# Kernel optimization log

Hardware: AMD Instinct MI355X
Metric: run time of the kernel (lower is better)

The kernel has to match this reference:

```python
import jax, jax.numpy as jnp
import numpy as np

B, C, H, W = 8, 256, 48, 48
CK = 64  # C // k
WSCALE = 0.3 / np.sqrt(C)  # keep exp(QK^T) finite (original has no 1/sqrt(d) scaling)


def conv1x1(x, w, b):
    # x: (B,C,H,W), w: (O,C,1,1), b: (O,) -> (B,O,H,W)
    return jnp.einsum('bchw,oc->bohw', x, w[:, :, 0, 0]) + b[None, :, None, None]


def setup_inputs() -> dict:
    key = jax.random.key(0)
    ks = jax.random.split(key, 6)
    x = jax.random.normal(ks[0], (B, C, H, W), dtype=jnp.float32)
    qw = jax.random.normal(ks[1], (CK, C, 1, 1), dtype=jnp.float32) * WSCALE
    kw = jax.random.normal(ks[2], (CK, C, 1, 1), dtype=jnp.float32) * WSCALE
    vw = jax.random.normal(ks[3], (C, C, 1, 1), dtype=jnp.float32) * (1.0 / np.sqrt(C))
    gw = jax.random.normal(ks[4], (C, C, 1, 1), dtype=jnp.float32) * (1.0 / np.sqrt(C))
    zk = jnp.zeros((CK,), dtype=jnp.float32)
    zc = jnp.zeros((C,), dtype=jnp.float32)
    return {
        'x': x,
        'query_weight': qw, 'query_bias': zk,
        'key_weight': kw, 'key_bias': zk,
        'value_weight': vw, 'value_bias': zc,
        'gamma_weight': gw, 'gamma_bias': zc,
        'k': 4,
    }


def reference(x, query_weight, query_bias, key_weight, key_bias,
              value_weight, value_bias, gamma_weight, gamma_bias, k):
    b, c, h, w = x.shape
    n = h * w
    q = conv1x1(x, query_weight, query_bias).reshape(b, -1, n)   # (B,Ck,N)
    kk = conv1x1(x, key_weight, key_bias).reshape(b, -1, n)      # (B,Ck,N)
    # energy[b,i,j] = q_i . k_j  (queries on rows, no sqrt(d) scaling)
    energy = jnp.einsum('bci,bcj->bij', q, kk)                   # (B,N,N)
    energy = jnp.exp(energy)
    energy = energy / jnp.sum(energy, axis=2, keepdims=True)     # unnormalized-softmax over keys
    v = conv1x1(x, value_weight, value_bias).reshape(b, c, n)    # (B,C,N)
    # out[b,c,j] = sum_i v[b,c,i] * energy[b,i,j]  (faithful to torch.bmm(V, energy))
    out = jnp.einsum('bci,bij->bcj', v, energy).reshape(b, c, h, w)
    out = conv1x1(out, gamma_weight, gamma_bias)
    return out
```

## Files before the change

### kernel.cpp

```cpp
#include <hip/hip_runtime.h>

#define BATCH 8
#define CIN   256
#define NPIX  2304
#define CKD   64
#define NIT   (NPIX / 16)
#define NIC   (NPIX / 32)
#define NJB   (NPIX / 64)

typedef _Float16 f16;
typedef __attribute__((ext_vector_type(4))) _Float16 f16x4;
typedef __attribute__((ext_vector_type(8))) _Float16 f16x8;
typedef __attribute__((ext_vector_type(4))) float    f32x4;


__global__ __launch_bounds__(256) void cast_w(
    const float* __restrict__ qw, const float* __restrict__ kw,
    const float* __restrict__ vw, const float* __restrict__ gw,
    f16* __restrict__ Wqk, f16* __restrict__ Wv, f16* __restrict__ Wg)
{
    int idx = (blockIdx.x * 256 + threadIdx.x) * 4;
    const float* src;
    f16* dst;
    if (idx < 16384)      { src = qw + idx;           dst = Wqk + idx; }
    else if (idx < 32768) { src = kw + (idx - 16384); dst = Wqk + idx; }
    else if (idx < 98304) { src = vw + (idx - 32768); dst = Wv + (idx - 32768); }
    else                  { src = gw + (idx - 98304); dst = Wg + (idx - 98304); }
    float4 v = *(const float4*)src;
    f16x4 h = { (f16)v.x, (f16)v.y, (f16)v.z, (f16)v.w };
    *(f16x4*)dst = h;
}

__global__ __launch_bounds__(256) void cast_xT(
    const float* __restrict__ x, f16* __restrict__ xT)
{
    __shared__ float s[64][65];
    const int t = threadIdx.x;
    const int n0 = blockIdx.x * 64, c0 = blockIdx.y * 64, b = blockIdx.z;
    const float* xb = x + ((size_t)b * CIN + c0) * NPIX + n0;

    const int cl = t >> 4, ng = (t & 15) * 4;
    #pragma unroll
    for (int p = 0; p < 4; ++p) {
        float4 v = *(const float4*)(xb + (size_t)(cl + 16 * p) * NPIX + ng);
        s[cl + 16 * p][ng + 0] = v.x;
        s[cl + 16 * p][ng + 1] = v.y;
        s[cl + 16 * p][ng + 2] = v.z;
        s[cl + 16 * p][ng + 3] = v.w;
    }
    __syncthreads();
    const int nl = t >> 2, cs = (t & 3) * 16;
    f16 h[16];
    #pragma unroll
    for (int j = 0; j < 16; ++j) h[j] = (f16)s[cs + j][nl];
    f16* gp = &xT[((size_t)b * NPIX + n0 + nl) * CIN + c0 + cs];
    *(f16x8*)gp       = *(f16x8*)&h[0];
    *(f16x8*)(gp + 8) = *(f16x8*)&h[8];
}

__global__ __launch_bounds__(256) void qk_conv_mfma(
    const f16* __restrict__ xT, const f16* __restrict__ Wqk,
    const float* __restrict__ qbias, const float* __restrict__ kbias,
    f16* __restrict__ q_blk, f16* __restrict__ k_blk)
{
    __shared__ __align__(16) f16 us[32 * 136];
    const int t = threadIdx.x, w = t >> 6, lane = t & 63;
    const int quad = lane >> 4, l16 = lane & 15;
    const int wm = w & 1, wn = w >> 1;
    const int n0 = blockIdx.x * 32, b = blockIdx.y;

    const f16* bp = xT + ((size_t)b * NPIX + n0 + 16 * wn + l16) * CIN;
    const f16* ap = Wqk + (size_t)(64 * wm + l16) * CIN;

    f32x4 acc[4];
    #pragma unroll
    for (int mt = 0; mt < 4; ++mt) acc[mt] = (f32x4){0.f, 0.f, 0.f, 0.f};

    #pragma unroll
    for (int kk = 0; kk < CIN; kk += 32) {
        f16x8 bf = *(const f16x8*)(bp + kk + quad * 8);
        #pragma unroll
        for (int mt = 0; mt < 4; ++mt) {
            f16x8 af = *(const f16x8*)(ap + (size_t)mt * 16 * CIN + kk + quad * 8);
            acc[mt] = __builtin_amdgcn_mfma_f32_16x16x32_f16(af, bf, acc[mt], 0, 0, 0);
        }
    }
    const float* bias = wm ? kbias - 64 : qbias;
    #pragma unroll
    for (int mt = 0; mt < 4; ++mt) {
        int ob = 64 * wm + 16 * mt + quad * 4;
        #pragma unroll
        for (int r = 0; r < 4; ++r)
            us[(16 * wn + l16) * 136 + ob + r] = (f16)(acc[mt][r] + bias[ob + r]);
    }
    __syncthreads();
    {
        int ks2 = t >> 7, nt = (t >> 6) & 1, ln = t & 63;
        const f16* usr = &us[(nt * 16 + (ln & 15)) * 136 + ks2 * 32 + (ln >> 4) * 8];
        size_t base = (((size_t)b * NIT + (n0 >> 4) + nt) * 2 + ks2) * 512 + ln * 8;
        *(f16x8*)&q_blk[base] = *(const f16x8*)(usr);
        *(f16x8*)&k_blk[base] = *(const f16x8*)(usr + 64);
    }
}

#define ESL 136
__global__ __launch_bounds__(256) void energy_S(
    const f16* __restrict__ q_blk, const f16* __restrict__ k_blk,
    float* __restrict__ Pred)
{
    __shared__ __align__(16) f16 es[64 * ESL];
    __shared__ float red2[2][128];
    const int t    = threadIdx.x;
    const int w    = t >> 6, lane = t & 63;
    const int quad = lane >> 4, l16 = lane & 15;
    const int j0 = blockIdx.x * 64, i0 = blockIdx.y * 128, b = blockIdx.z;
    const size_t ln8 = (size_t)lane * 8;
    const f16* qb = q_blk + (size_t)b * NIT * 2 * 512 + ln8;

    f32x4 acc[8];
    #pragma unroll
    for (int mt = 0; mt < 8; ++mt) acc[mt] = (f32x4){0.f, 0.f, 0.f, 0.f};

    #pragma unroll
    for (int ks = 0; ks < 2; ++ks) {
        f16x8 bf = *(const f16x8*)(k_blk +
            (((size_t)b * NIT + (j0 >> 4) + w) * 2 + ks) * 512 + ln8);
        #pragma unroll
        for (int mt = 0; mt < 8; ++mt) {
            f16x8 af = *(const f16x8*)(qb + ((size_t)((i0 >> 4) + mt) * 2 + ks) * 512);
            acc[mt] = __builtin_amdgcn_mfma_f32_16x16x32_f16(af, bf, acc[mt], 0, 0, 0);
        }
    }

    #pragma unroll
    for (int mt = 0; mt < 8; ++mt) {
        f16x4 h = { (f16)__expf(acc[mt][0]), (f16)__expf(acc[mt][1]),
                    (f16)__expf(acc[mt][2]), (f16)__expf(acc[mt][3]) };
        *(f16x4*)&es[(16 * w + l16) * ESL + 16 * mt + quad * 4] = h;
    }
    __syncthreads();
    {
        int i = t & 127, jq = t >> 7;
        float s = 0.f;
        #pragma unroll
        for (int jj = 0; jj < 32; ++jj)
            s += (float)es[(jq * 32 + jj) * ESL + i];
        red2[jq][i] = s;
    }
    __syncthreads();
    if (t < 128)
        Pred[((size_t)blockIdx.x * BATCH + b) * NPIX + i0 + t] =
            red2[0][t] + red2[1][t];
}

__global__ __launch_bounds__(256) void reduce_S(
    const float* __restrict__ Pred, float* __restrict__ S)
{
    const size_t BN = (size_t)BATCH * NPIX;
    size_t idx = (size_t)blockIdx.x * 256 + threadIdx.x;
    float s = 0.f;
    #pragma unroll
    for (int jb = 0; jb < NJB; ++jb)
        s += Pred[(size_t)jb * BN + idx];
    S[idx] = s;
}

__global__ __launch_bounds__(256) void v_conv_mfma(
    const f16* __restrict__ xT, const f16* __restrict__ Wv,
    const float* __restrict__ vbias, const float* __restrict__ S,
    f16* __restrict__ u_blk)
{
    __shared__ __align__(16) f16 smem[9216];
    f16* As = smem;
    f16* Bs = smem + 128 * 40;
    f16* us = smem;
    const int t = threadIdx.x, w = t >> 6, lane = t & 63;
    const int quad = lane >> 4, l16 = lane & 15;
    const int wm = w & 1, wn = w >> 1;
    const int i0 = blockIdx.x * 64, c0 = blockIdx.y * 128, b = blockIdx.z;
    const int sub = t >> 2, le = t & 3;
    const f16* srcA = Wv + (size_t)(c0 + sub) * CIN + le * 8;
    const f16* srcB = xT + ((size_t)b * NPIX + i0 + sub) * CIN + le * 8;
    const int ldsw = sub * 40 + le * 8;

    f32x4 acc[4][2];
    #pragma unroll
    for (int mt = 0; mt < 4; ++mt)
        #pragma unroll
        for (int nt = 0; nt < 2; ++nt)
            acc[mt][nt] = (f32x4){0.f, 0.f, 0.f, 0.f};

    for (int kk = 0; kk < CIN; kk += 32) {
        f16x8 ta0 = *(const f16x8*)(srcA + kk);
        f16x8 ta1 = *(const f16x8*)(srcA + (size_t)64 * CIN + kk);
        f16x8 tb0 = *(const f16x8*)(srcB + kk);
        __syncthreads();
        *(f16x8*)&As[ldsw]           = ta0;
        *(f16x8*)&As[64 * 40 + ldsw] = ta1;
        *(f16x8*)&Bs[ldsw]           = tb0;
        __syncthreads();
        f16x8 af[4], bf[2];
        #pragma unroll
        for (int mt = 0; mt < 4; ++mt)
            af[mt] = *(const f16x8*)&As[(64 * wm + 16 * mt + l16) * 40 + quad * 8];
        #pragma unroll
        for (int nt = 0; nt < 2; ++nt)
            bf[nt] = *(const f16x8*)&Bs[(32 * wn + 16 * nt + l16) * 40 + quad * 8];
        #pragma unroll
        for (int mt = 0; mt < 4; ++mt)
            #pragma unroll
            for (int nt = 0; nt < 2; ++nt)
                acc[mt][nt] = __builtin_amdgcn_mfma_f32_16x16x32_f16(
                    af[mt], bf[nt], acc[mt][nt], 0, 0, 0);
    }

    __syncthreads();
    #pragma unroll
    for (int nt = 0; nt < 2; ++nt) {
        int i = 32 * wn + 16 * nt + l16;
        float is = 1.0f / S[(size_t)b * NPIX + i0 + i];
        #pragma unroll
        for (int mt = 0; mt < 4; ++mt)
            #pragma unroll
            for (int r = 0; r < 4; ++r) {
                int c = 64 * wm + 16 * mt + quad * 4 + r;
                us[c * 72 + i] = (f16)((acc[mt][nt][r] + vbias[c0 + c]) * is);
            }
    }
    __syncthreads();
    #pragma unroll
    for (int p = 0; p < 4; ++p) {
        int g  = t + 256 * p;
        int ct = g >> 7, ic = (g >> 6) & 1, ln = g & 63;
        f16x8 v = *(const f16x8*)&us[(ct * 16 + (ln & 15)) * 72 + ic * 32 + (ln >> 4) * 8];
        *(f16x8*)&u_blk[(((size_t)b * 16 + (c0 >> 4) + ct) * NIC + (i0 >> 5) + ic) * 512 + ln * 8] = v;
    }
}

__global__ __launch_bounds__(256) void fused_bmm(
    const f16* __restrict__ q_blk, const f16* __restrict__ k_blk,
    const f16* __restrict__ u_blk, f16* __restrict__ o1T)
{
    __shared__ __align__(16) f16 es[64 * 72];
    const int t = threadIdx.x, w = t >> 6, lane = t & 63;
    const int quad = lane >> 4, l16 = lane & 15;
    const int j0 = blockIdx.x * 64;
    const int ch = blockIdx.y, b = blockIdx.z;
    const size_t ln8 = (size_t)lane * 8;

    const f16* qb = q_blk + (size_t)b * NIT * 2 * 512 + ln8;
    const f16* ub = u_blk + (size_t)b * 16 * NIC * 512 + ln8;

    f16x8 kf[2];
    #pragma unroll
    for (int ks = 0; ks < 2; ++ks)
        kf[ks] = *(const f16x8*)(k_blk +
            (((size_t)b * NIT + (j0 >> 4) + w) * 2 + ks) * 512 + ln8);

    const int CT0 = ch * 8 + 2 * w;

    f32x4 acc[2][4];
    #pragma unroll
    for (int mt = 0; mt < 2; ++mt)
        #pragma unroll
        for (int jt = 0; jt < 4; ++jt)
            acc[mt][jt] = (f32x4){0.f, 0.f, 0.f, 0.f};

    for (int ic = 0; ic < NPIX / 64; ++ic) {
        f32x4 e[4];
        #pragma unroll
        for (int it = 0; it < 4; ++it) e[it] = (f32x4){0.f, 0.f, 0.f, 0.f};
        #pragma unroll
        for (int ks = 0; ks < 2; ++ks)
            #pragma unroll
            for (int it = 0; it < 4; ++it) {
                f16x8 af = *(const f16x8*)(qb + ((size_t)(ic * 4 + it) * 2 + ks) * 512);
                e[it] = __builtin_amdgcn_mfma_f32_16x16x32_f16(af, kf[ks], e[it], 0, 0, 0);
            }
        __syncthreads();
        #pragma unroll
        for (int it = 0; it < 4; ++it) {
            f16x4 h = { (f16)__expf(e[it][0]), (f16)__expf(e[it][1]),
                        (f16)__expf(e[it][2]), (f16)__expf(e[it][3]) };
            *(f16x4*)&es[(16 * w + l16) * 72 + it * 16 + quad * 4] = h;
        }
        __syncthreads();
        #pragma unroll
        for (int isub = 0; isub < 2; ++isub) {
            f16x8 af0 = *(const f16x8*)(ub + ((size_t)(CT0 + 0) * NIC + ic * 2 + isub) * 512);
            f16x8 af1 = *(const f16x8*)(ub + ((size_t)(CT0 + 1) * NIC + ic * 2 + isub) * 512);
            #pragma unroll
            for (int jt = 0; jt < 4; ++jt) {
                f16x8 bf = *(const f16x8*)&es[(16 * jt + l16) * 72 + isub * 32 + quad * 8];
                acc[0][jt] = __builtin_amdgcn_mfma_f32_16x16x32_f16(af0, bf, acc[0][jt], 0, 0, 0);
                acc[1][jt] = __builtin_amdgcn_mfma_f32_16x16x32_f16(af1, bf, acc[1][jt], 0, 0, 0);
            }
        }
    }

    #pragma unroll
    for (int mt = 0; mt < 2; ++mt) {
        int cb = ch * 128 + 32 * w + 16 * mt + quad * 4;
        #pragma unroll
        for (int jt = 0; jt < 4; ++jt) {
            int j = j0 + 16 * jt + l16;
            f16x4 h = { (f16)acc[mt][jt][0], (f16)acc[mt][jt][1],
                        (f16)acc[mt][jt][2], (f16)acc[mt][jt][3] };
            *(f16x4*)&o1T[((size_t)b * NPIX + j) * CIN + cb] = h;
        }
    }
}

__global__ __launch_bounds__(256) void gamma_conv_mfma(
    const f16* __restrict__ o1T, const f16* __restrict__ Wg,
    const float* __restrict__ gbias, float* __restrict__ out)
{
    __shared__ __align__(16) f16 As[128 * 40];
    __shared__ __align__(16) f16 Bs[64 * 40];
    const int t = threadIdx.x, w = t >> 6, lane = t & 63;
    const int quad = lane >> 4, l16 = lane & 15;
    const int wm = w & 1, wn = w >> 1;
    const int j0 = blockIdx.x * 64, o0 = blockIdx.y * 128, b = blockIdx.z;
    const int sub = t >> 2, le = t & 3;
    const f16* srcA = Wg + (size_t)(o0 + sub) * CIN + le * 8;
    const f16* srcB = o1T + ((size_t)b * NPIX + j0 + sub) * CIN + le * 8;
    const int ldsw = sub * 40 + le * 8;

    f32x4 acc[4][2];
    #pragma unroll
    for (int mt = 0; mt < 4; ++mt)
        #pragma unroll
        for (int nt = 0; nt < 2; ++nt)
            acc[mt][nt] = (f32x4){0.f, 0.f, 0.f, 0.f};

    for (int kk = 0; kk < CIN; kk += 32) {
        f16x8 ta0 = *(const f16x8*)(srcA + kk);
        f16x8 ta1 = *(const f16x8*)(srcA + (size_t)64 * CIN + kk);
        f16x8 tb0 = *(const f16x8*)(srcB + kk);
        __syncthreads();
        *(f16x8*)&As[ldsw]           = ta0;
        *(f16x8*)&As[64 * 40 + ldsw] = ta1;
        *(f16x8*)&Bs[ldsw]           = tb0;
        __syncthreads();
        f16x8 af[4], bf[2];
        #pragma unroll
        for (int mt = 0; mt < 4; ++mt)
            af[mt] = *(const f16x8*)&As[(64 * wm + 16 * mt + l16) * 40 + quad * 8];
        #pragma unroll
        for (int nt = 0; nt < 2; ++nt)
            bf[nt] = *(const f16x8*)&Bs[(32 * wn + 16 * nt + l16) * 40 + quad * 8];
        #pragma unroll
        for (int mt = 0; mt < 4; ++mt)
            #pragma unroll
            for (int nt = 0; nt < 2; ++nt)
                acc[mt][nt] = __builtin_amdgcn_mfma_f32_16x16x32_f16(
                    af[mt], bf[nt], acc[mt][nt], 0, 0, 0);
    }

    #pragma unroll
    for (int mt = 0; mt < 4; ++mt)
        #pragma unroll
        for (int r = 0; r < 4; ++r) {
            int o = o0 + 64 * wm + 16 * mt + quad * 4 + r;
            float bv = gbias[o];
            #pragma unroll
            for (int nt = 0; nt < 2; ++nt) {
                int j = j0 + 32 * wn + 16 * nt + l16;
                out[((size_t)b * CIN + o) * NPIX + j] = acc[mt][nt][r] + bv;
            }
        }
}

extern "C" void kernel_launch(void* const* d_in, const int* in_sizes, int n_in,
                              void* d_out, int out_size, void* d_ws, size_t ws_size,
                              hipStream_t stream) {
    const float* x   = (const float*)d_in[0];
    const float* qw  = (const float*)d_in[1];
    const float* qbv = (const float*)d_in[2];
    const float* kw  = (const float*)d_in[3];
    const float* kbv = (const float*)d_in[4];
    const float* vw  = (const float*)d_in[5];
    const float* vbv = (const float*)d_in[6];
    const float* gw  = (const float*)d_in[7];
    const float* gbv = (const float*)d_in[8];
    float* out = (float*)d_out;

    const size_t BCN  = (size_t)BATCH * CIN * NPIX;
    const size_t BN   = (size_t)BATCH * NPIX;
    const size_t BNCK = (size_t)BATCH * NPIX * CKD;

    f16* q_blk = (f16*)d_ws;
    f16* k_blk = q_blk + BNCK;
    f16* u_blk = k_blk + BNCK;
    f16* xT    = u_blk + BCN;
    f16* o1T   = xT + BCN;
    f16* Wqk   = o1T + BCN;
    f16* Wv    = Wqk + 128 * 256;
    f16* Wg    = Wv + 256 * 256;
    float* S   = (float*)(Wg + 256 * 256);
    float* Pred= S + BN;

    cast_w<<<160, 256, 0, stream>>>(qw, kw, vw, gw, Wqk, Wv, Wg);
    cast_xT<<<dim3(NPIX / 64, CIN / 64, BATCH), 256, 0, stream>>>(x, xT);
    qk_conv_mfma<<<dim3(NPIX / 32, BATCH), 256, 0, stream>>>(xT, Wqk, qbv, kbv, q_blk, k_blk);
    energy_S<<<dim3(NPIX / 64, NPIX / 128, BATCH), 256, 0, stream>>>(q_blk, k_blk, Pred);
    reduce_S<<<(int)(BN / 256), 256, 0, stream>>>(Pred, S);
    v_conv_mfma<<<dim3(NPIX / 64, CIN / 128, BATCH), 256, 0, stream>>>(xT, Wv, vbv, S, u_blk);
    fused_bmm<<<dim3(NPIX / 64, 2, BATCH), 256, 0, stream>>>(q_blk, k_blk, u_blk, o1T);
    gamma_conv_mfma<<<dim3(NPIX / 64, CIN / 128, BATCH), 256, 0, stream>>>(o1T, Wg, gbv, out);
}
```

Before: 209.5 us.

## Restructure fused_bmm to 512-thread blocks covering all channels per 32-column tile

The fused energy/value kernel now uses 512-thread blocks that each cover all 256 channels for a 32-column j tile, instead of two channel halves over 64 columns. Each exp(energy) tile is computed once per block rather than once per channel half, which removes the duplicated QK^T and exp work. The energy tile is stored in a double-buffered LDS layout that matches the MFMA fragment order, so one barrier per iteration is enough. The cost is a smaller j tile, so each K fragment feeds less work, and a larger block that may limit occupancy and scheduling flexibility.

```diff
diff --git a/kernel.cpp b/kernel.cpp
--- a/kernel.cpp
+++ b/kernel.cpp
@@ -237,61 +237,59 @@
     }
 }
 
-__global__ __launch_bounds__(256) void fused_bmm(
+__global__ __launch_bounds__(512) void fused_bmm(
     const f16* __restrict__ q_blk, const f16* __restrict__ k_blk,
     const f16* __restrict__ u_blk, f16* __restrict__ o1T)
 {
-    __shared__ __align__(16) f16 es[64 * 72];
+    __shared__ __align__(16) f16 es[2][4][512];
     const int t = threadIdx.x, w = t >> 6, lane = t & 63;
     const int quad = lane >> 4, l16 = lane & 15;
-    const int j0 = blockIdx.x * 64;
-    const int ch = blockIdx.y, b = blockIdx.z;
+    const int j0 = blockIdx.x * 32;
+    const int b = blockIdx.y;
     const size_t ln8 = (size_t)lane * 8;
 
     const f16* qb = q_blk + (size_t)b * NIT * 2 * 512 + ln8;
     const f16* ub = u_blk + (size_t)b * 16 * NIC * 512 + ln8;
 
+    const int jt1 = w & 1;
+    const int iw  = w >> 1;
+
     f16x8 kf[2];
     #pragma unroll
     for (int ks = 0; ks < 2; ++ks)
         kf[ks] = *(const f16x8*)(k_blk +
-            (((size_t)b * NIT + (j0 >> 4) + w) * 2 + ks) * 512 + ln8);
-
-    const int CT0 = ch * 8 + 2 * w;
-
-    f32x4 acc[2][4];
+            (((size_t)b * NIT + (j0 >> 4) + jt1) * 2 + ks) * 512 + ln8);
+
+    const int CT0 = w * 2;
+    const int etile = jt1 * 2 + (iw >> 1);
+    const int woff  = ((iw & 1) * 2 + (quad >> 1)) * 128 + l16 * 8 + (quad & 1) * 4;
+
+    f32x4 acc[2][2];
     #pragma unroll
     for (int mt = 0; mt < 2; ++mt)
         #pragma unroll
-        for (int jt = 0; jt < 4; ++jt)
+        for (int jt = 0; jt < 2; ++jt)
             acc[mt][jt] = (f32x4){0.f, 0.f, 0.f, 0.f};
 
     for (int ic = 0; ic < NPIX / 64; ++ic) {
-        f32x4 e[4];
-        #pragma unroll
-        for (int it = 0; it < 4; ++it) e[it] = (f32x4){0.f, 0.f, 0.f, 0.f};
-        #pragma unroll
-        for (int ks = 0; ks < 2; ++ks)
-            #pragma unroll
-            for (int it = 0; it < 4; ++it) {
-                f16x8 af = *(const f16x8*)(qb + ((size_t)(ic * 4 + it) * 2 + ks) * 512);
-                e[it] = __builtin_amdgcn_mfma_f32_16x16x32_f16(af, kf[ks], e[it], 0, 0, 0);
-            }
-        __syncthreads();
-        #pragma unroll
-        for (int it = 0; it < 4; ++it) {
-            f16x4 h = { (f16)__expf(e[it][0]), (f16)__expf(e[it][1]),
-                        (f16)__expf(e[it][2]), (f16)__expf(e[it][3]) };
-            *(f16x4*)&es[(16 * w + l16) * 72 + it * 16 + quad * 4] = h;
-        }
+        const int cur = ic & 1;
+        f32x4 e = (f32x4){0.f, 0.f, 0.f, 0.f};
+        #pragma unroll
+        for (int ks = 0; ks < 2; ++ks) {
+            f16x8 af = *(const f16x8*)(qb + ((size_t)(ic * 4 + iw) * 2 + ks) * 512);
+            e = __builtin_amdgcn_mfma_f32_16x16x32_f16(af, kf[ks], e, 0, 0, 0);
+        }
+        f16x4 h = { (f16)__expf(e[0]), (f16)__expf(e[1]),
+                    (f16)__expf(e[2]), (f16)__expf(e[3]) };
+        *(f16x4*)&es[cur][etile][woff] = h;
         __syncthreads();
         #pragma unroll
         for (int isub = 0; isub < 2; ++isub) {
             f16x8 af0 = *(const f16x8*)(ub + ((size_t)(CT0 + 0) * NIC + ic * 2 + isub) * 512);
             f16x8 af1 = *(const f16x8*)(ub + ((size_t)(CT0 + 1) * NIC + ic * 2 + isub) * 512);
             #pragma unroll
-            for (int jt = 0; jt < 4; ++jt) {
-                f16x8 bf = *(const f16x8*)&es[(16 * jt + l16) * 72 + isub * 32 + quad * 8];
+            for (int jt = 0; jt < 2; ++jt) {
+                f16x8 bf = *(const f16x8*)&es[cur][jt * 2 + isub][ln8];
                 acc[0][jt] = __builtin_amdgcn_mfma_f32_16x16x32_f16(af0, bf, acc[0][jt], 0, 0, 0);
                 acc[1][jt] = __builtin_amdgcn_mfma_f32_16x16x32_f16(af1, bf, acc[1][jt], 0, 0, 0);
             }
@@ -300,13 +298,13 @@
 
     #pragma unroll
     for (int mt = 0; mt < 2; ++mt) {
-        int cb = ch * 128 + 32 * w + 16 * mt + quad * 4;
-        #pragma unroll
-        for (int jt = 0; jt < 4; ++jt) {
+        int cb = 32 * w + 16 * mt + quad * 4;
+        #pragma unroll
+        for (int jt = 0; jt < 2; ++jt) {
             int j = j0 + 16 * jt + l16;
-            f16x4 h = { (f16)acc[mt][jt][0], (f16)acc[mt][jt][1],
-                        (f16)acc[mt][jt][2], (f16)acc[mt][jt][3] };
-            *(f16x4*)&o1T[((size_t)b * NPIX + j) * CIN + cb] = h;
+            f16x4 h2 = { (f16)acc[mt][jt][0], (f16)acc[mt][jt][1],
+                         (f16)acc[mt][jt][2], (f16)acc[mt][jt][3] };
+            *(f16x4*)&o1T[((size_t)b * NPIX + j) * CIN + cb] = h2;
         }
     }
 }
@@ -406,6 +404,6 @@
     energy_S<<<dim3(NPIX / 64, NPIX / 128, BATCH), 256, 0, stream>>>(q_blk, k_blk, Pred);
     reduce_S<<<(int)(BN / 256), 256, 0, stream>>>(Pred, S);
     v_conv_mfma<<<dim3(NPIX / 64, CIN / 128, BATCH), 256, 0, stream>>>(xT, Wv, vbv, S, u_blk);
-    fused_bmm<<<dim3(NPIX / 64, 2, BATCH), 256, 0, stream>>>(q_blk, k_blk, u_blk, o1T);
+    fused_bmm<<<dim3(NPIX / 32, BATCH), 512, 0, stream>>>(q_blk, k_blk, u_blk, o1T);
     gamma_conv_mfma<<<dim3(NPIX / 64, CIN / 128, BATCH), 256, 0, stream>>>(o1T, Wg, gbv, out);
 }
```

Measured after the change: 198.4 us. 1.06x faster.
